# Optimization experiments

Hardware: AMD Instinct MI355X
Metric: run time of the kernel (lower is better)

The kernel has to match this reference:

```python
import jax, jax.numpy as jnp
import numpy as np

B, OBS, ACT, NT, E, H1, H2, D = 4096, 390, 20, 10, 8, 1024, 512, 256


def setup_inputs() -> dict:
    key = jax.random.key(0)
    ks = jax.random.split(key, 16)
    f32 = jnp.float32

    def w(k, shape, fan_in):
        return jax.random.normal(k, shape, f32) / np.float32(np.sqrt(fan_in))

    return {
        "state_feat": jax.random.normal(ks[0], (B, OBS), f32),
        "act": jax.random.normal(ks[1], (B, ACT), f32),
        "task_id": jax.random.randint(ks[2], (B,), 0, NT, jnp.int32),
        "rep_W1": w(ks[3], (OBS + ACT, H1), OBS + ACT),
        "rep_b1": jnp.zeros((H1,), f32),
        "rep_W2": w(ks[4], (H1, H1), H1),
        "rep_b2": jnp.zeros((H1,), f32),
        "emb": 0.5 * jax.random.normal(ks[5], (NT, D), f32),
        "kW1": w(ks[6], (E, H1, H2), H1),
        "kb1": jnp.zeros((E, H2), f32),
        "kW2": w(ks[7], (E, H2, D), H2),
        "kb2": jnp.zeros((E, D), f32),
        "vW1": w(ks[8], (E, H1, H2), H1),
        "vb1": jnp.zeros((E, H2), f32),
        "vW2": w(ks[9], (E, H2, D), H2),
        "vb2": jnp.zeros((E, D), f32),
        "tW1": w(ks[10], (D, D), D),
        "tb1": jnp.zeros((D,), f32),
        "tW2": w(ks[11], (D, D), D),
        "tb2": jnp.zeros((D,), f32),
        "tW3": w(ks[12], (D, 1), D),
        "tb3": jnp.zeros((1,), f32),
    }


def reference(state_feat, act, task_id, rep_W1, rep_b1, rep_W2, rep_b2, emb,
              kW1, kb1, kW2, kb2, vW1, vb1, vW2, vb2,
              tW1, tb1, tW2, tb2, tW3, tb3):
    # representation: mlp([obs+act, 1024, 1024]) -> ReLU on first layer only
    x = jnp.concatenate([state_feat, act], axis=-1)              # [B, 410]
    rep = jnp.maximum(x @ rep_W1 + rep_b1, 0.0) @ rep_W2 + rep_b2  # [B, H1]
    query = jnp.tanh(emb[task_id])                               # [B, D]

    # batched per-expert key/value MLPs (grouped GEMM instead of python loop)
    hk = jnp.maximum(jnp.einsum('bi,eio->ebo', rep, kW1) + kb1[:, None, :], 0.0)
    keys = jnp.einsum('ebo,eod->ebd', hk, kW2) + kb2[:, None, :]   # [E, B, D]
    hv = jnp.maximum(jnp.einsum('bi,eio->ebo', rep, vW1) + vb1[:, None, :], 0.0)
    vals = jnp.einsum('ebo,eod->ebd', hv, vW2) + vb2[:, None, :]   # [E, B, D]

    scores = jnp.einsum('bd,ebd->be', query, keys)               # [B, E]
    weight = jax.nn.softmax(scores, axis=1)                      # [B, E]
    tower_in = jnp.einsum('be,ebd->bd', weight, vals)            # [B, D]

    # tower: mlp([256, 256, 256, 1]) -> ReLU, ReLU, Identity
    h = jnp.maximum(tower_in @ tW1 + tb1, 0.0)
    h = jnp.maximum(h @ tW2 + tb2, 0.0)
    q = (h @ tW3 + tb3)[:, 0]                                    # [B]

    expert_loss = -jnp.mean(
        jnp.sum(jnp.clip(jnp.log(weight + 1e-10), -6.0, 0.0), axis=-1) * 0.3)
    return q, expert_loss
```

## Files before the change

kernel.cpp:

```cpp
#include <hip/hip_runtime.h>

constexpr int Bn   = 4096;
constexpr int OBS  = 390;
constexpr int ACTN = 20;
constexpr int IN   = 410;
constexpr int KPAD = 448;
constexpr int E    = 8;
constexpr int NT   = 10;
constexpr int H1   = 1024;
constexpr int H2   = 512;
constexpr int D    = 256;

typedef __bf16 bf16x8 __attribute__((ext_vector_type(8)));
typedef float  f32x4  __attribute__((ext_vector_type(4)));
typedef unsigned short u16x8 __attribute__((ext_vector_type(8)));

__device__ __forceinline__ unsigned short f2bf(float f) {
    unsigned int u = __float_as_uint(f);
    unsigned int r = u + 0x7fffu + ((u >> 16) & 1u);
    return (unsigned short)(r >> 16);
}
__device__ __forceinline__ float bf2f(unsigned short h) {
    return __uint_as_float(((unsigned int)h) << 16);
}
__device__ __forceinline__ void gload16(void* lds_dst, const void* g_src) {
    __builtin_amdgcn_global_load_lds(
        (const __attribute__((address_space(1))) void*)g_src,
        (__attribute__((address_space(3))) void*)lds_dst,
        16, 0, 0);
}

struct TD2 {
    const float* W;
    unsigned short* WT;
    int K, Kpad, N;
    long long gsW, gsO;
    int tilesN, perG, start;
};
struct TD2Arr { TD2 d[8]; };

__global__ __launch_bounds__(256) void tc64(TD2Arr da) {
    int bid = blockIdx.x;
    int i = 0;
#pragma unroll
    for (int j = 1; j < 8; ++j) if (bid >= da.d[j].start) i = j;
    TD2 dd = da.d[i];
    int local = bid - dd.start;
    int g   = local / dd.perG;
    int rem = local - g * dd.perG;
    int kt  = rem / dd.tilesN;
    int nt  = rem - kt * dd.tilesN;
    const float* W = dd.W + (long long)g * dd.gsW;
    unsigned short* WT = dd.WT + (long long)g * dd.gsO;
    int k0 = kt * 64, n0 = nt * 64;

    __shared__ float tile[64][68];
    int t = threadIdx.x;
    {
        int kl  = t >> 4;
        int nl4 = (t & 15) * 4;
#pragma unroll
        for (int r = 0; r < 4; ++r) {
            int k = k0 + kl + r * 16;
            float4 v = make_float4(0.f, 0.f, 0.f, 0.f);
            if (k < dd.K) v = *(const float4*)(W + (long long)k * dd.N + n0 + nl4);
            *(float4*)&tile[kl + r * 16][nl4] = v;
        }
    }
    __syncthreads();
    int nl = t >> 2, kc = (t & 3) * 16;
    if (k0 + kc < dd.Kpad) {
        u16x8 o0, o1;
#pragma unroll
        for (int j = 0; j < 8; ++j) {
            o0[j] = f2bf(tile[kc + j][nl]);
            o1[j] = f2bf(tile[kc + 8 + j][nl]);
        }
        unsigned short* dst = WT + (long long)(n0 + nl) * dd.Kpad + k0 + kc;
        *(u16x8*)dst       = o0;
        *(u16x8*)(dst + 8) = o1;
    }
}

constexpr int PREPB = (Bn * KPAD) / 256;

__global__ __launch_bounds__(256) void misc_kernel(
    const float* __restrict__ sf, const float* __restrict__ ac,
    unsigned short* __restrict__ x,
    const float* __restrict__ kW2, const float* __restrict__ kb2,
    const float* __restrict__ emb, float* __restrict__ qp, float* __restrict__ qb,
    const float* __restrict__ kb1, const float* __restrict__ vb1,
    float* __restrict__ b1cat)
{
    int bid = blockIdx.x;
    if (bid < PREPB) {
        int idx = bid * 256 + threadIdx.x;
        int b = idx / KPAD;
        int k = idx - b * KPAD;
        float v = 0.f;
        if (k < OBS) v = sf[b * OBS + k];
        else if (k < IN) v = ac[b * ACTN + (k - OBS)];
        x[idx] = f2bf(v);
        return;
    }
    if (bid < PREPB + 17) {
        int qbid = bid - PREPB;
        __shared__ float tq[NT][D];
        for (int i = threadIdx.x; i < NT * D; i += 256)
            tq[i / D][i - (i / D) * D] = tanhf(emb[i]);
        __syncthreads();
        if (qbid < 16) {
            int e = qbid >> 1;
            int h = (qbid & 1) * 256 + threadIdx.x;
            const float4* row = (const float4*)(kW2 + ((long long)e * H2 + h) * D);
            float acc[NT] = {};
            for (int d4 = 0; d4 < D / 4; ++d4) {
                float4 wv = row[d4];
#pragma unroll
                for (int t = 0; t < NT; ++t)
                    acc[t] += wv.x * tq[t][d4 * 4] + wv.y * tq[t][d4 * 4 + 1]
                            + wv.z * tq[t][d4 * 4 + 2] + wv.w * tq[t][d4 * 4 + 3];
            }
#pragma unroll
            for (int t = 0; t < NT; ++t)
                qp[((long long)e * NT + t) * H2 + h] = acc[t];
        } else if (threadIdx.x < E * NT) {
            int e = threadIdx.x / NT, t = threadIdx.x - e * NT;
            float s = 0.f;
            for (int d = 0; d < D; ++d) s += kb2[e * D + d] * tq[t][d];
            qb[e * NT + t] = s;
        }
        return;
    }
    int i = (bid - PREPB - 17) * 256 + threadIdx.x;
    b1cat[i] = (i < E * H2) ? kb1[i] : vb1[i - E * H2];
}

template <int ACTF, int OUTF, int BK>
__global__ __launch_bounds__(256) void gemm_bf16(
    const unsigned short* __restrict__ A, const unsigned short* __restrict__ BT,
    const float* __restrict__ bias, void* __restrict__ Cout,
    int K, int ldc,
    long long gsA, long long gsBT, long long gsBias, long long gsC,
    const float* __restrict__ tW3 = nullptr, float* __restrict__ qpart = nullptr)
{
    constexpr int CH   = BK / 8;
    constexpr int RPR  = 256 / CH;
    constexpr int RNDS = 128 / RPR;
    constexpr int TB   = 128 * BK * 2;
    constexpr int RS   = CH * 16;

    const int g = blockIdx.z;
    A    += (long long)g * gsA;
    BT   += (long long)g * gsBT;
    bias += (long long)g * gsBias;
    float*          Cf = (float*)Cout + (long long)g * gsC;
    unsigned short* Cb = (unsigned short*)Cout + (long long)g * gsC;

    __shared__ alignas(16) char smem[2 * TB];
    const int t  = threadIdx.x;
    const int w  = t >> 6, l = t & 63;
    const int lr = l & 15, lk = l >> 4;
    const int gm = blockIdx.y * 128, gn = blockIdx.x * 128;
    const int wm = (w >> 1) * 64,   wn = (w & 1) * 64;

    const int srow = t / CH;
    const int swzS = (CH == 8) ? (srow & 7) : ((srow >> 1) & 3);
    const int sc   = (t % CH) ^ swzS;
    const unsigned short* gA = A  + (long long)(gm + srow) * K + sc * 8;
    const unsigned short* gB = BT + (long long)(gn + srow) * K + sc * 8;

    const int swzL = (CH == 8) ? (lr & 7) : ((lr >> 1) & 3);
    const int aoff = (wm + lr) * RS + ((lk ^ swzL) * 16);
    const int boff = TB + (wn + lr) * RS + ((lk ^ swzL) * 16);

    f32x4 acc[4][4] = {};

    for (int k0 = 0; k0 < K; k0 += BK) {
#pragma unroll
        for (int j = 0; j < RNDS; ++j) {
            gload16(smem + j * 4096 + w * 1024,      gA + k0 + (long long)j * RPR * K);
            gload16(smem + TB + j * 4096 + w * 1024, gB + k0 + (long long)j * RPR * K);
        }
        __syncthreads();

        bf16x8 af[4], bfr[4];
#pragma unroll
        for (int i = 0; i < 4; ++i) {
            af[i]  = *(const bf16x8*)(smem + aoff + i * 16 * RS);
            bfr[i] = *(const bf16x8*)(smem + boff + i * 16 * RS);
        }
#pragma unroll
        for (int mi = 0; mi < 4; ++mi)
#pragma unroll
            for (int ni = 0; ni < 4; ++ni)
                acc[mi][ni] = __builtin_amdgcn_mfma_f32_16x16x32_bf16(
                    af[mi], bfr[ni], acc[mi][ni], 0, 0, 0);

        if constexpr (BK == 64) {
#pragma unroll
            for (int i = 0; i < 4; ++i) {
                af[i]  = *(const bf16x8*)(smem + (aoff ^ 64) + i * 16 * RS);
                bfr[i] = *(const bf16x8*)(smem + (boff ^ 64) + i * 16 * RS);
            }
#pragma unroll
            for (int mi = 0; mi < 4; ++mi)
#pragma unroll
                for (int ni = 0; ni < 4; ++ni)
                    acc[mi][ni] = __builtin_amdgcn_mfma_f32_16x16x32_bf16(
                        af[mi], bfr[ni], acc[mi][ni], 0, 0, 0);
        }
        __syncthreads();
    }

    const int orow0 = gm + wm + lk * 4;
    const int ocol0 = gn + wn + lr;
    float bv[4];
#pragma unroll
    for (int ni = 0; ni < 4; ++ni) bv[ni] = bias[gn + wn + lr + ni * 16];

    if (OUTF == 2) {
        float tw3v[4];
#pragma unroll
        for (int ni = 0; ni < 4; ++ni) tw3v[ni] = tW3[gn + wn + lr + ni * 16];
#pragma unroll
        for (int mi = 0; mi < 4; ++mi)
#pragma unroll
            for (int r = 0; r < 4; ++r) {
                float part = 0.f;
#pragma unroll
                for (int ni = 0; ni < 4; ++ni) {
                    float v = acc[mi][ni][r] + bv[ni];
                    if (ACTF == 1) v = fmaxf(v, 0.f);
                    part += v * tw3v[ni];
                }
                part += __shfl_xor(part, 1);
                part += __shfl_xor(part, 2);
                part += __shfl_xor(part, 4);
                part += __shfl_xor(part, 8);
                if (lr == 0)
                    qpart[(orow0 + mi * 16 + r) * 4 + ((wn >> 6) << 1) + blockIdx.x] = part;
            }
    } else {
#pragma unroll
        for (int mi = 0; mi < 4; ++mi)
#pragma unroll
            for (int ni = 0; ni < 4; ++ni)
#pragma unroll
                for (int r = 0; r < 4; ++r) {
                    float v = acc[mi][ni][r] + bv[ni];
                    if (ACTF == 1) v = fmaxf(v, 0.f);
                    long long off = (long long)(orow0 + mi * 16 + r) * ldc + ocol0 + ni * 16;
                    if (OUTF == 0) Cf[off] = v;
                    else           Cb[off] = f2bf(v);
                }
    }
}

template <int KTOT, int ACTF, int OUTF, int SC>
__global__ __launch_bounds__(512, 2) void gemm256(
    const unsigned short* __restrict__ A, const unsigned short* __restrict__ BT,
    const float* __restrict__ bias, void* __restrict__ Cout,
    int ldc, long long gsA, long long gsBT, long long gsBias, long long gsC,
    const int* __restrict__ task_id, const float* __restrict__ qp,
    float* __restrict__ spart)
{
    constexpr int NT_ = KTOT / 64;
    static_assert(NT_ >= 4 && (NT_ % 2) == 0, "KTOT must be multiple of 128");

    const int g = blockIdx.z;
    A    += (long long)g * gsA;
    BT   += (long long)g * gsBT;
    bias += (long long)g * gsBias;
    float*          Cf = (float*)Cout + (long long)g * gsC;
    unsigned short* Cb = (unsigned short*)Cout + (long long)g * gsC;

    __shared__ __align__(16) char smem[131072];

    const int tid = threadIdx.x;
    const int l  = tid & 63;
    const int lr = l & 15, lk = l >> 4;
    const int w  = tid >> 6;
    const int wr = w >> 2, wc = w & 3;
    const int gm = blockIdx.y * 256, gn = blockIdx.x * 256;

    const int srow = tid >> 3;
    const int cg   = (tid & 7) ^ (srow & 7);
    const unsigned short* gA = A  + (long long)(gm + srow) * KTOT + cg * 8;
    const unsigned short* gB = BT + (long long)(gn + srow) * KTOT + cg * 8;
    const int wbase = (tid & ~63) * 16;

    const int cs0 = ((0 | lk) ^ (lr & 7)) * 16;
    const int cs1 = ((4 | lk) ^ (lr & 7)) * 16;
    const int aRow = wr * 16384 + lr * 128;
    const int bRow = 32768 + (wc >> 1) * 16384 + ((wc & 1) * 64 + lr) * 128;

    f32x4 acc[8][4] = {};

    auto stA = [&](int c, int s, int kt) {
        const unsigned short* src = gA + (long long)(s * 128) * KTOT + kt * 64;
        char* d = smem + c * 65536 + s * 16384 + wbase;
        gload16(d,        src);
        gload16(d + 8192, src + (long long)64 * KTOT);
    };
    auto stB = [&](int c, int s, int kt) {
        const unsigned short* src = gB + (long long)(s * 128) * KTOT + kt * 64;
        char* d = smem + c * 65536 + 32768 + s * 16384 + wbase;
        gload16(d,        src);
        gload16(d + 8192, src + (long long)64 * KTOT);
    };

    stA(0, 0, 0); stA(0, 1, 0); stB(0, 0, 0); stB(0, 1, 0);
    stA(1, 0, 1); stA(1, 1, 1);
    asm volatile("s_waitcnt vmcnt(4)" ::: "memory");
    __builtin_amdgcn_s_barrier();
    __builtin_amdgcn_sched_barrier(0);

#pragma unroll
    for (int kt = 0; kt < NT_; ++kt) {
        const int c = kt & 1;
        const char* bufc = smem + c * 65536;
        bf16x8 a0[4], a1[4], b0[4], b1[4];

#pragma unroll
        for (int m = 0; m < 4; ++m) {
            const char* base = bufc + aRow + m * (16 * 128);
            a0[m] = *(const bf16x8*)(base + cs0);
            a1[m] = *(const bf16x8*)(base + cs1);
        }
#pragma unroll
        for (int n = 0; n < 4; ++n) {
            const char* base = bufc + bRow + n * (16 * 128);
            b0[n] = *(const bf16x8*)(base + cs0);
            b1[n] = *(const bf16x8*)(base + cs1);
        }
        if (kt + 1 < NT_) { stB(c ^ 1, 0, kt + 1); stB(c ^ 1, 1, kt + 1); }
        __builtin_amdgcn_s_setprio(1);
#pragma unroll
        for (int m = 0; m < 4; ++m)
#pragma unroll
            for (int n = 0; n < 4; ++n) {
                acc[m][n] = __builtin_amdgcn_mfma_f32_16x16x32_bf16(a0[m], b0[n], acc[m][n], 0, 0, 0);
                acc[m][n] = __builtin_amdgcn_mfma_f32_16x16x32_bf16(a1[m], b1[n], acc[m][n], 0, 0, 0);
            }
        __builtin_amdgcn_s_setprio(0);

#pragma unroll
        for (int m = 0; m < 4; ++m) {
            const char* base = bufc + aRow + (64 + m * 16) * 128;
            a0[m] = *(const bf16x8*)(base + cs0);
            a1[m] = *(const bf16x8*)(base + cs1);
        }
        asm volatile("s_waitcnt lgkmcnt(0)" ::: "memory");
        __builtin_amdgcn_sched_barrier(0);
        if (kt + 2 < NT_) {
            __builtin_amdgcn_s_barrier();
            __builtin_amdgcn_sched_barrier(0);
            stA(c, 0, kt + 2); stA(c, 1, kt + 2);
        }
        __builtin_amdgcn_s_setprio(1);
#pragma unroll
        for (int m = 0; m < 4; ++m)
#pragma unroll
            for (int n = 0; n < 4; ++n) {
                acc[4 + m][n] = __builtin_amdgcn_mfma_f32_16x16x32_bf16(a0[m], b0[n], acc[4 + m][n], 0, 0, 0);
                acc[4 + m][n] = __builtin_amdgcn_mfma_f32_16x16x32_bf16(a1[m], b1[n], acc[4 + m][n], 0, 0, 0);
            }
        __builtin_amdgcn_s_setprio(0);

        if (kt + 1 < NT_) {
            if (kt + 2 < NT_) { asm volatile("s_waitcnt vmcnt(4)" ::: "memory"); }
            else              { asm volatile("s_waitcnt vmcnt(0)" ::: "memory"); }
            __builtin_amdgcn_sched_barrier(0);
            __builtin_amdgcn_s_barrier();
            __builtin_amdgcn_sched_barrier(0);
        }
    }

    const int orow0 = gm + wr * 128 + lk * 4;
    const int ocol0 = gn + wc * 64 + lr;
    float bv[4];
#pragma unroll
    for (int ni = 0; ni < 4; ++ni) bv[ni] = bias[gn + wc * 64 + lr + ni * 16];

    if (SC && g < E) {
        __syncthreads();
        float* qpl  = (float*)smem;
        int*   tidl = (int*)(smem + NT * 256 * 4);
        for (int i = tid; i < NT * 256; i += 512) {
            int tt = i >> 8, cc = i & 255;
            qpl[i] = qp[((long long)(g * NT + tt)) * H2 + gn + cc];
        }
        if (tid < 256) tidl[tid] = task_id[gm + tid];
        __syncthreads();

        const int rbase = wr * 128 + lk * 4;
        const int cbase = wc * 64 + lr;
#pragma unroll
        for (int mi = 0; mi < 8; ++mi) {
#pragma unroll
            for (int r = 0; r < 4; ++r) {
                int trow = tidl[rbase + mi * 16 + r];
                float rp = 0.f;
#pragma unroll
                for (int ni = 0; ni < 4; ++ni) {
                    float v = acc[mi][ni][r] + bv[ni];
                    v = fmaxf(v, 0.f);
                    rp += v * qpl[trow * 256 + cbase + ni * 16];
                }
                rp += __shfl_xor(rp, 1);
                rp += __shfl_xor(rp, 2);
                rp += __shfl_xor(rp, 4);
                rp += __shfl_xor(rp, 8);
                if (lr == 0)
                    spart[(((long long)g * Bn + orow0 + mi * 16 + r) << 3)
                          + (wc << 1) + blockIdx.x] = rp;
            }
        }
    } else {
#pragma unroll
        for (int mi = 0; mi < 8; ++mi)
#pragma unroll
            for (int ni = 0; ni < 4; ++ni)
#pragma unroll
                for (int r = 0; r < 4; ++r) {
                    float v = acc[mi][ni][r] + bv[ni];
                    if (ACTF == 1) v = fmaxf(v, 0.f);
                    long long off = (long long)(orow0 + mi * 16 + r) * ldc + ocol0 + ni * 16;
                    if (OUTF == 0) Cf[off] = v;
                    else           Cb[off] = f2bf(v);
                }
    }
}

__global__ __launch_bounds__(256) void attn_kernel(
    const float* __restrict__ spart, const float* __restrict__ qb,
    const int* __restrict__ task_id, const unsigned short* __restrict__ vals,
    unsigned short* __restrict__ tower_in, float* __restrict__ loss_partial)
{
    int wv   = threadIdx.x >> 6;
    int lane = threadIdx.x & 63;
    int b    = blockIdx.x * 4 + wv;
    int t    = task_id[b];

    float s[E];
#pragma unroll
    for (int e = 0; e < E; ++e) {
        const float4* sp = (const float4*)(spart + (((long long)e * Bn + b) << 3));
        float4 p0 = sp[0], p1 = sp[1];
        s[e] = p0.x + p0.y + p0.z + p0.w + p1.x + p1.y + p1.z + p1.w + qb[e * NT + t];
    }

    float m = s[0];
#pragma unroll
    for (int e = 1; e < E; ++e) m = fmaxf(m, s[e]);
    float wgt[E];
    float sum = 0.f;
#pragma unroll
    for (int e = 0; e < E; ++e) { wgt[e] = expf(s[e] - m); sum += wgt[e]; }
    float inv = 1.f / sum;

    int d0 = lane * 4;
    float4 acc = make_float4(0.f, 0.f, 0.f, 0.f);
    float lb = 0.f;
#pragma unroll
    for (int e = 0; e < E; ++e) {
        float we = wgt[e] * inv;
        uint2 vv = *(const uint2*)&vals[((long long)e * Bn + b) * D + d0];
        acc.x += we * __uint_as_float(vv.x << 16);
        acc.y += we * __uint_as_float(vv.x & 0xffff0000u);
        acc.z += we * __uint_as_float(vv.y << 16);
        acc.w += we * __uint_as_float(vv.y & 0xffff0000u);
        lb += fminf(fmaxf(logf(we + 1e-10f), -6.f), 0.f);
    }
    ushort4 o;
    o.x = f2bf(acc.x); o.y = f2bf(acc.y); o.z = f2bf(acc.z); o.w = f2bf(acc.w);
    *(ushort4*)&tower_in[(long long)b * D + d0] = o;

    __shared__ float sm[4];
    if (lane == 0) sm[wv] = lb;
    __syncthreads();
    if (threadIdx.x == 0)
        loss_partial[blockIdx.x] = sm[0] + sm[1] + sm[2] + sm[3];
}

__global__ __launch_bounds__(256) void qfin_kernel(
    const float* __restrict__ qpart, const float* __restrict__ tb3,
    float* __restrict__ out, const float* __restrict__ lossp)
{
    if (blockIdx.x == Bn / 256) {
        float s = 0.f;
        for (int i = threadIdx.x; i < Bn / 4; i += 256) s += lossp[i];
#pragma unroll
        for (int off = 32; off > 0; off >>= 1) s += __shfl_xor(s, off, 64);
        __shared__ float sm[4];
        if ((threadIdx.x & 63) == 0) sm[threadIdx.x >> 6] = s;
        __syncthreads();
        if (threadIdx.x == 0) out[Bn] = (-0.3f / Bn) * (sm[0] + sm[1] + sm[2] + sm[3]);
        return;
    }
    int b = blockIdx.x * 256 + threadIdx.x;
    float4 qpv = *(const float4*)&qpart[b * 4];
    out[b] = qpv.x + qpv.y + qpv.z + qpv.w + tb3[0];
}

extern "C" void kernel_launch(void* const* d_in, const int* in_sizes, int n_in,
                              void* d_out, int out_size, void* d_ws, size_t ws_size,
                              hipStream_t stream) {
    const float* state_feat = (const float*)d_in[0];
    const float* act        = (const float*)d_in[1];
    const int*   task_id    = (const int*)d_in[2];
    const float* rep_W1 = (const float*)d_in[3];
    const float* rep_b1 = (const float*)d_in[4];
    const float* rep_W2 = (const float*)d_in[5];
    const float* rep_b2 = (const float*)d_in[6];
    const float* emb    = (const float*)d_in[7];
    const float* kW1 = (const float*)d_in[8];
    const float* kb1 = (const float*)d_in[9];
    const float* kW2 = (const float*)d_in[10];
    const float* kb2 = (const float*)d_in[11];
    const float* vW1 = (const float*)d_in[12];
    const float* vb1 = (const float*)d_in[13];
    const float* vW2 = (const float*)d_in[14];
    const float* vb2 = (const float*)d_in[15];
    const float* tW1 = (const float*)d_in[16];
    const float* tb1 = (const float*)d_in[17];
    const float* tW2 = (const float*)d_in[18];
    const float* tb2 = (const float*)d_in[19];
    const float* tW3 = (const float*)d_in[20];
    const float* tb3 = (const float*)d_in[21];
    float* out = (float*)d_out;

    char* p = (char*)d_ws;
    auto alloc = [&](size_t bytes) {
        char* r = p;
        p += (bytes + 255) & ~(size_t)255;
        return r;
    };
    unsigned short* x      = (unsigned short*)alloc((size_t)Bn * KPAD * 2);
    unsigned short* repW1T = (unsigned short*)alloc((size_t)H1 * KPAD * 2);
    unsigned short* repW2T = (unsigned short*)alloc((size_t)H1 * H1 * 2);
    unsigned short* w1T    = (unsigned short*)alloc((size_t)2 * E * H2 * H1 * 2);
    unsigned short* w2T    = (unsigned short*)alloc((size_t)E * D * H2 * 2);
    unsigned short* tW1T   = (unsigned short*)alloc((size_t)D * D * 2);
    unsigned short* tW2T   = (unsigned short*)alloc((size_t)D * D * 2);
    float*          b1cat  = (float*)alloc((size_t)2 * E * H2 * 4);
    float*          qp     = (float*)alloc((size_t)E * NT * H2 * 4);
    float*          qb     = (float*)alloc((size_t)E * NT * 4);
    char*           h1zone = alloc((size_t)Bn * H1 * 2);
    unsigned short* rep    = (unsigned short*)alloc((size_t)Bn * H1 * 2);
    unsigned short* hkv    = (unsigned short*)alloc((size_t)2 * E * Bn * H2 * 2);
    unsigned short* vals   = (unsigned short*)alloc((size_t)E * Bn * D * 2);
    float*          spart  = (float*)alloc((size_t)E * Bn * 8 * 4);
    float*          qpart  = (float*)alloc((size_t)Bn * 4 * 4);
    float*          lossp  = (float*)alloc((size_t)(Bn / 4) * 4);

    unsigned short* h1       = (unsigned short*)h1zone;
    unsigned short* tower_in = (unsigned short*)h1zone;
    unsigned short* t1       = (unsigned short*)(h1zone + (size_t)Bn * D * 2);
    unsigned short* hv = hkv + (size_t)E * Bn * H2;

    TD2Arr da;
    int startAcc = 0;
    auto setd = [&](int i, const float* W, unsigned short* WT, int K, int Kpad, int N,
                    long long gsW, long long gsO, int groups) {
        TD2& dd = da.d[i];
        dd.W = W; dd.WT = WT; dd.K = K; dd.Kpad = Kpad; dd.N = N;
        dd.gsW = gsW; dd.gsO = gsO;
        dd.tilesN = N / 64;
        dd.perG = ((Kpad + 63) / 64) * dd.tilesN;
        dd.start = startAcc;
        startAcc += dd.perG * groups;
    };
    setd(0, rep_W1, repW1T, IN, KPAD, H1, 0, 0, 1);
    setd(1, rep_W2, repW2T, H1, H1, H1, 0, 0, 1);
    setd(2, kW1, w1T,                       H1, H1, H2, (long long)H1 * H2, (long long)H2 * H1, E);
    setd(3, vW1, w1T + (size_t)E * H2 * H1, H1, H1, H2, (long long)H1 * H2, (long long)H2 * H1, E);
    setd(4, vW2, w2T,                       H2, H2, D, (long long)H2 * D, (long long)D * H2, E);
    setd(5, tW1, tW1T, D, D, D, 0, 0, 1);
    setd(6, tW2, tW2T, D, D, D, 0, 0, 1);
    da.d[7] = da.d[6];
    da.d[7].start = 0x7fffffff;
    tc64<<<startAcc, 256, 0, stream>>>(da);

    misc_kernel<<<PREPB + 17 + 32, 256, 0, stream>>>(
        state_feat, act, x, kW2, kb2, emb, qp, qb, kb1, vb1, b1cat);

    gemm_bf16<1, 1, 64><<<dim3(H1 / 128, Bn / 128, 1), 256, 0, stream>>>(
        x, repW1T, rep_b1, h1, KPAD, H1, 0, 0, 0, 0);
    gemm_bf16<0, 1, 64><<<dim3(H1 / 128, Bn / 128, 1), 256, 0, stream>>>(
        h1, repW2T, rep_b2, rep, H1, H1, 0, 0, 0, 0);

    gemm256<H1, 1, 1, 1><<<dim3(H2 / 256, Bn / 256, 2 * E), 512, 0, stream>>>(
        rep, w1T, b1cat, hkv, H2,
        0, (long long)H2 * H1, H2, (long long)Bn * H2,
        task_id, qp, spart);
    gemm_bf16<0, 1, 64><<<dim3(D / 128, Bn / 128, E), 256, 0, stream>>>(
        hv, w2T, vb2, vals, H2, D,
        (long long)Bn * H2, (long long)D * H2, D, (long long)Bn * D);

    attn_kernel<<<Bn / 4, 256, 0, stream>>>(
        spart, qb, task_id, vals, tower_in, lossp);

    gemm_bf16<1, 1, 64><<<dim3(D / 128, Bn / 128, 1), 256, 0, stream>>>(
        tower_in, tW1T, tb1, t1, D, D, 0, 0, 0, 0);
    gemm_bf16<1, 2, 64><<<dim3(D / 128, Bn / 128, 1), 256, 0, stream>>>(
        t1, tW2T, tb2, nullptr, D, D, 0, 0, 0, 0, tW3, qpart);

    qfin_kernel<<<Bn / 256 + 1, 256, 0, stream>>>(qpart, tb3, out, lossp);
}
```

Baseline: 179.3 us.

## Double-buffer 128x128 bf16 GEMM with split-phase prefetch and compile-time K

```diff
diff --git a/kernel.cpp b/kernel.cpp
--- a/kernel.cpp
+++ b/kernel.cpp
@@ -136,19 +136,15 @@
     b1cat[i] = (i < E * H2) ? kb1[i] : vb1[i - E * H2];
 }
 
-template <int ACTF, int OUTF, int BK>
-__global__ __launch_bounds__(256) void gemm_bf16(
+template <int KT, int ACTF, int OUTF>
+__global__ __launch_bounds__(256, 2) void gemm128p(
     const unsigned short* __restrict__ A, const unsigned short* __restrict__ BT,
     const float* __restrict__ bias, void* __restrict__ Cout,
-    int K, int ldc,
-    long long gsA, long long gsBT, long long gsBias, long long gsC,
+    int ldc, long long gsA, long long gsBT, long long gsBias, long long gsC,
     const float* __restrict__ tW3 = nullptr, float* __restrict__ qpart = nullptr)
 {
-    constexpr int CH   = BK / 8;
-    constexpr int RPR  = 256 / CH;
-    constexpr int RNDS = 128 / RPR;
-    constexpr int TB   = 128 * BK * 2;
-    constexpr int RS   = CH * 16;
+    constexpr int NTK = KT / 64;
+    static_assert(NTK >= 2, "KT must be >= 128");
 
     const int g = blockIdx.z;
     A    += (long long)g * gsA;
@@ -157,60 +153,105 @@
     float*          Cf = (float*)Cout + (long long)g * gsC;
     unsigned short* Cb = (unsigned short*)Cout + (long long)g * gsC;
 
-    __shared__ alignas(16) char smem[2 * TB];
-    const int t  = threadIdx.x;
-    const int w  = t >> 6, l = t & 63;
-    const int lr = l & 15, lk = l >> 4;
+    __shared__ __align__(16) char smem[65536];
+    const int tid = threadIdx.x;
+    const int l  = tid & 63, lr = l & 15, lk = l >> 4;
+    const int w  = tid >> 6;
+    const int wm = (w >> 1) * 64, wn = (w & 1) * 64;
     const int gm = blockIdx.y * 128, gn = blockIdx.x * 128;
-    const int wm = (w >> 1) * 64,   wn = (w & 1) * 64;
-
-    const int srow = t / CH;
-    const int swzS = (CH == 8) ? (srow & 7) : ((srow >> 1) & 3);
-    const int sc   = (t % CH) ^ swzS;
-    const unsigned short* gA = A  + (long long)(gm + srow) * K + sc * 8;
-    const unsigned short* gB = BT + (long long)(gn + srow) * K + sc * 8;
-
-    const int swzL = (CH == 8) ? (lr & 7) : ((lr >> 1) & 3);
-    const int aoff = (wm + lr) * RS + ((lk ^ swzL) * 16);
-    const int boff = TB + (wn + lr) * RS + ((lk ^ swzL) * 16);
+
+    const int srow = tid >> 3;
+    const int cg   = (tid & 7) ^ (srow & 7);
+    const unsigned short* gA = A  + (long long)(gm + srow) * KT + cg * 8;
+    const unsigned short* gB = BT + (long long)(gn + srow) * KT + cg * 8;
+    const int wb = w * 1024;
+
+    const int cs0 = ((0 | lk) ^ (lr & 7)) * 16;
+    const int cs1 = ((4 | lk) ^ (lr & 7)) * 16;
+    const int aRow = (wm + lr) * 128;
+    const int bRow = 16384 + (wn + lr) * 128;
 
     f32x4 acc[4][4] = {};
 
-    for (int k0 = 0; k0 < K; k0 += BK) {
-#pragma unroll
-        for (int j = 0; j < RNDS; ++j) {
-            gload16(smem + j * 4096 + w * 1024,      gA + k0 + (long long)j * RPR * K);
-            gload16(smem + TB + j * 4096 + w * 1024, gB + k0 + (long long)j * RPR * K);
-        }
-        __syncthreads();
-
-        bf16x8 af[4], bfr[4];
-#pragma unroll
-        for (int i = 0; i < 4; ++i) {
-            af[i]  = *(const bf16x8*)(smem + aoff + i * 16 * RS);
-            bfr[i] = *(const bf16x8*)(smem + boff + i * 16 * RS);
-        }
-#pragma unroll
-        for (int mi = 0; mi < 4; ++mi)
-#pragma unroll
-            for (int ni = 0; ni < 4; ++ni)
-                acc[mi][ni] = __builtin_amdgcn_mfma_f32_16x16x32_bf16(
-                    af[mi], bfr[ni], acc[mi][ni], 0, 0, 0);
-
-        if constexpr (BK == 64) {
-#pragma unroll
-            for (int i = 0; i < 4; ++i) {
-                af[i]  = *(const bf16x8*)(smem + (aoff ^ 64) + i * 16 * RS);
-                bfr[i] = *(const bf16x8*)(smem + (boff ^ 64) + i * 16 * RS);
-            }
-#pragma unroll
-            for (int mi = 0; mi < 4; ++mi)
-#pragma unroll
-                for (int ni = 0; ni < 4; ++ni)
-                    acc[mi][ni] = __builtin_amdgcn_mfma_f32_16x16x32_bf16(
-                        af[mi], bfr[ni], acc[mi][ni], 0, 0, 0);
-        }
-        __syncthreads();
+    auto stA = [&](int c, int kt) {
+#pragma unroll
+        for (int j = 0; j < 4; ++j)
+            gload16(smem + c * 32768 + j * 4096 + wb,
+                    gA + (long long)(j * 32) * KT + kt * 64);
+    };
+    auto stB = [&](int c, int kt) {
+#pragma unroll
+        for (int j = 0; j < 4; ++j)
+            gload16(smem + c * 32768 + 16384 + j * 4096 + wb,
+                    gB + (long long)(j * 32) * KT + kt * 64);
+    };
+
+    stA(0, 0); stB(0, 0); stA(1, 1);
+    asm volatile("s_waitcnt vmcnt(4)" ::: "memory");
+    __builtin_amdgcn_s_barrier();
+    __builtin_amdgcn_sched_barrier(0);
+
+#pragma unroll
+    for (int kt = 0; kt < NTK; ++kt) {
+        const int c = kt & 1;
+        const char* bufc = smem + c * 32768;
+        bf16x8 a[4][2], b[2][2], b2[2][2];
+
+#pragma unroll
+        for (int m = 0; m < 4; ++m) {
+            const char* base = bufc + aRow + m * 2048;
+            a[m][0] = *(const bf16x8*)(base + cs0);
+            a[m][1] = *(const bf16x8*)(base + cs1);
+        }
+#pragma unroll
+        for (int n = 0; n < 2; ++n) {
+            const char* base = bufc + bRow + n * 2048;
+            b[n][0] = *(const bf16x8*)(base + cs0);
+            b[n][1] = *(const bf16x8*)(base + cs1);
+        }
+        if (kt + 1 < NTK) stB(c ^ 1, kt + 1);
+        __builtin_amdgcn_s_setprio(1);
+#pragma unroll
+        for (int ks = 0; ks < 2; ++ks)
+#pragma unroll
+            for (int m = 0; m < 4; ++m)
+#pragma unroll
+                for (int n = 0; n < 2; ++n)
+                    acc[m][n] = __builtin_amdgcn_mfma_f32_16x16x32_bf16(
+                        a[m][ks], b[n][ks], acc[m][n], 0, 0, 0);
+        __builtin_amdgcn_s_setprio(0);
+
+#pragma unroll
+        for (int n = 0; n < 2; ++n) {
+            const char* base = bufc + bRow + (2 + n) * 2048;
+            b2[n][0] = *(const bf16x8*)(base + cs0);
+            b2[n][1] = *(const bf16x8*)(base + cs1);
+        }
+        asm volatile("s_waitcnt lgkmcnt(0)" ::: "memory");
+        __builtin_amdgcn_sched_barrier(0);
+        if (kt + 2 < NTK) {
+            __builtin_amdgcn_s_barrier();
+            __builtin_amdgcn_sched_barrier(0);
+            stA(c, kt + 2);
+        }
+        __builtin_amdgcn_s_setprio(1);
+#pragma unroll
+        for (int ks = 0; ks < 2; ++ks)
+#pragma unroll
+            for (int m = 0; m < 4; ++m)
+#pragma unroll
+                for (int n = 0; n < 2; ++n)
+                    acc[m][2 + n] = __builtin_amdgcn_mfma_f32_16x16x32_bf16(
+                        a[m][ks], b2[n][ks], acc[m][2 + n], 0, 0, 0);
+        __builtin_amdgcn_s_setprio(0);
+
+        if (kt + 1 < NTK) {
+            if (kt + 2 < NTK) { asm volatile("s_waitcnt vmcnt(4)" ::: "memory"); }
+            else              { asm volatile("s_waitcnt vmcnt(0)" ::: "memory"); }
+            __builtin_amdgcn_sched_barrier(0);
+            __builtin_amdgcn_s_barrier();
+            __builtin_amdgcn_sched_barrier(0);
+        }
     }
 
     const int orow0 = gm + wm + lk * 4;
@@ -586,26 +627,26 @@
     misc_kernel<<<PREPB + 17 + 32, 256, 0, stream>>>(
         state_feat, act, x, kW2, kb2, emb, qp, qb, kb1, vb1, b1cat);
 
-    gemm_bf16<1, 1, 64><<<dim3(H1 / 128, Bn / 128, 1), 256, 0, stream>>>(
-        x, repW1T, rep_b1, h1, KPAD, H1, 0, 0, 0, 0);
-    gemm_bf16<0, 1, 64><<<dim3(H1 / 128, Bn / 128, 1), 256, 0, stream>>>(
-        h1, repW2T, rep_b2, rep, H1, H1, 0, 0, 0, 0);
+    gemm128p<KPAD, 1, 1><<<dim3(H1 / 128, Bn / 128, 1), 256, 0, stream>>>(
+        x, repW1T, rep_b1, h1, H1, 0, 0, 0, 0);
+    gemm128p<H1, 0, 1><<<dim3(H1 / 128, Bn / 128, 1), 256, 0, stream>>>(
+        h1, repW2T, rep_b2, rep, H1, 0, 0, 0, 0);
 
     gemm256<H1, 1, 1, 1><<<dim3(H2 / 256, Bn / 256, 2 * E), 512, 0, stream>>>(
         rep, w1T, b1cat, hkv, H2,
         0, (long long)H2 * H1, H2, (long long)Bn * H2,
         task_id, qp, spart);
-    gemm_bf16<0, 1, 64><<<dim3(D / 128, Bn / 128, E), 256, 0, stream>>>(
-        hv, w2T, vb2, vals, H2, D,
+    gemm128p<H2, 0, 1><<<dim3(D / 128, Bn / 128, E), 256, 0, stream>>>(
+        hv, w2T, vb2, vals, D,
         (long long)Bn * H2, (long long)D * H2, D, (long long)Bn * D);
 
     attn_kernel<<<Bn / 4, 256, 0, stream>>>(
         spart, qb, task_id, vals, tower_in, lossp);
 
-    gemm_bf16<1, 1, 64><<<dim3(D / 128, Bn / 128, 1), 256, 0, stream>>>(
-        tower_in, tW1T, tb1, t1, D, D, 0, 0, 0, 0);
-    gemm_bf16<1, 2, 64><<<dim3(D / 128, Bn / 128, 1), 256, 0, stream>>>(
-        t1, tW2T, tb2, nullptr, D, D, 0, 0, 0, 0, tW3, qpart);
+    gemm128p<D, 1, 1><<<dim3(D / 128, Bn / 128, 1), 256, 0, stream>>>(
+        tower_in, tW1T, tb1, t1, D, 0, 0, 0, 0);
+    gemm128p<D, 1, 2><<<dim3(D / 128, Bn / 128, 1), 256, 0, stream>>>(
+        t1, tW2T, tb2, nullptr, D, 0, 0, 0, 0, tW3, qpart);
 
     qfin_kernel<<<Bn / 256 + 1, 256, 0, stream>>>(qpart, tb3, out, lossp);
 }
```

Measured after the change: 162.3 us. -9.5%, faster.
